# Kernel optimization log

Hardware: AMD Instinct MI355X
Metric: run time of the kernel (lower is better)

The kernel has to match this reference:

```python
import jax, jax.numpy as jnp
import numpy as np

D_MODEL = 1024
NUM_HEADS = 16
D_K = D_MODEL // NUM_HEADS


def setup_inputs() -> dict:
    key = jax.random.key(0)
    ks = jax.random.split(key, 12)
    B, L, D = 1, 4096, D_MODEL
    s = 1.0 / np.sqrt(D)
    return {
        "q": jax.random.normal(ks[0], (B, L, D), jnp.float32),
        "k": jax.random.normal(ks[1], (B, L, D), jnp.float32),
        "v": jax.random.normal(ks[2], (B, L, D), jnp.float32),
        "wq": jax.random.normal(ks[3], (D, D), jnp.float32) * s,
        "bq": jnp.zeros((D,), jnp.float32),
        "wk": jax.random.normal(ks[4], (D, D), jnp.float32) * s,
        "bk": jnp.zeros((D,), jnp.float32),
        "wv": jax.random.normal(ks[5], (D, D), jnp.float32) * s,
        "bv": jnp.zeros((D,), jnp.float32),
        "wo": jax.random.normal(ks[6], (D, D), jnp.float32) * s,
        "bo": jnp.zeros((D,), jnp.float32),
    }


def reference(q, k, v, wq, bq, wk, bk, wv, bv, wo, bo):
    B, L, D = q.shape
    H, dk = NUM_HEADS, D_K
    # linear projections then split heads: [B, L, D] -> [B, H, L, dk]
    def proj(x, w, b):
        return (x @ w.T + b).reshape(B, L, H, dk).transpose(0, 2, 1, 3)
    qh = proj(q, wq, bq)
    kh = proj(k, wk, bk)
    vh = proj(v, wv, bv)
    scores = jnp.einsum("bhqd,bhkd->bhqk", qh, kh) / jnp.sqrt(jnp.float32(dk))
    attn = jax.nn.softmax(scores, axis=-1)  # [B, H, L, L]
    out = jnp.einsum("bhqk,bhkd->bhqd", attn, vh)
    out = out.transpose(0, 2, 1, 3).reshape(B, L, D)
    return out @ wo.T + bo
```

## Files before the change

### kernel.cpp

```cpp
#include <hip/hip_runtime.h>
#include <hip/hip_bf16.h>
#include <stdint.h>


typedef __bf16 bf16_t;
typedef __bf16 bf16x8 __attribute__((ext_vector_type(8)));
typedef __bf16 bf16x4 __attribute__((ext_vector_type(4)));
typedef float f32x4 __attribute__((ext_vector_type(4)));
typedef unsigned short u16x8 __attribute__((ext_vector_type(8)));

#define MFMA_BF16 __builtin_amdgcn_mfma_f32_16x16x32_bf16

__device__ __forceinline__ void async_copy16(const void* g, void* lds) {
  __builtin_amdgcn_global_load_lds(
      (__attribute__((address_space(1))) void*)(uintptr_t)g,
      (__attribute__((address_space(3))) void*)lds, 16, 0, 0);
}

__global__ __launch_bounds__(256) void cast_f32_bf16(
    const float* __restrict__ s0, bf16_t* __restrict__ d0, int n0,
    const float* __restrict__ s1, bf16_t* __restrict__ d1, int n1,
    const float* __restrict__ s2, bf16_t* __restrict__ d2, int n2,
    const float* __restrict__ s3, bf16_t* __restrict__ d3, int n3,
    const float* __restrict__ s4, bf16_t* __restrict__ d4, int n4,
    const float* __restrict__ s5, bf16_t* __restrict__ d5, int n5,
    const float* __restrict__ s6, bf16_t* __restrict__ d6, int n6) {
  const float* s;
  bf16_t* d;
  int n;
  switch (blockIdx.z) {
    case 0: s = s0; d = d0; n = n0; break;
    case 1: s = s1; d = d1; n = n1; break;
    case 2: s = s2; d = d2; n = n2; break;
    case 3: s = s3; d = d3; n = n3; break;
    case 4: s = s4; d = d4; n = n4; break;
    case 5: s = s5; d = d5; n = n5; break;
    default: s = s6; d = d6; n = n6; break;
  }
  const int i = (blockIdx.x * 256 + threadIdx.x) * 8;
  if (i >= n) return;
  float4 a = *(const float4*)(s + i);
  float4 b = *(const float4*)(s + i + 4);
  bf16x8 o;
  o[0] = (bf16_t)a.x; o[1] = (bf16_t)a.y; o[2] = (bf16_t)a.z; o[3] = (bf16_t)a.w;
  o[4] = (bf16_t)b.x; o[5] = (bf16_t)b.y; o[6] = (bf16_t)b.z; o[7] = (bf16_t)b.w;
  *(bf16x8*)(d + i) = o;
}

template <typename CT>
__global__ __launch_bounds__(256) void gemm3_bt(
    const bf16_t* __restrict__ A0, const bf16_t* __restrict__ W0,
    const float* __restrict__ b0, CT* __restrict__ C0,
    const bf16_t* __restrict__ A1, const bf16_t* __restrict__ W1,
    const float* __restrict__ b1, CT* __restrict__ C1,
    const bf16_t* __restrict__ A2, const bf16_t* __restrict__ W2,
    const float* __restrict__ b2, CT* __restrict__ C2,
    int M, int N, int K) {
  const bf16_t *A, *W;
  const float* bias;
  CT* C;
  if (blockIdx.z == 0)      { A = A0; W = W0; bias = b0; C = C0; }
  else if (blockIdx.z == 1) { A = A1; W = W1; bias = b1; C = C1; }
  else                      { A = A2; W = W2; bias = b2; C = C2; }

  __shared__ bf16_t As[128][32];
  __shared__ bf16_t Bs[128][32];

  const int t = threadIdx.x;
  const int w = t >> 6, lane = t & 63;
  const int quad = lane >> 4, l16 = lane & 15;
  const int wr = w >> 1, wc = w & 1;
  const int m0 = blockIdx.x * 128;
  const int n0 = blockIdx.y * 128;
  const int srow = lane >> 2;
  const int scol = (lane & 3) * 8;

  f32x4 acc[4][4] = {};

  for (int k0 = 0; k0 < K; k0 += 32) {
    async_copy16(&A[(size_t)(m0 + (2 * w) * 16 + srow) * K + k0 + scol],
                 (char*)As + (2 * w) * 1024);
    async_copy16(&A[(size_t)(m0 + (2 * w + 1) * 16 + srow) * K + k0 + scol],
                 (char*)As + (2 * w + 1) * 1024);
    async_copy16(&W[(size_t)(n0 + (2 * w) * 16 + srow) * K + k0 + scol],
                 (char*)Bs + (2 * w) * 1024);
    async_copy16(&W[(size_t)(n0 + (2 * w + 1) * 16 + srow) * K + k0 + scol],
                 (char*)Bs + (2 * w + 1) * 1024);
    __syncthreads();

    bf16x8 af[4], bfr[4];
#pragma unroll
    for (int mt = 0; mt < 4; mt++)
      af[mt] = *(const bf16x8*)&As[wr * 64 + mt * 16 + l16][quad * 8];
#pragma unroll
    for (int nt = 0; nt < 4; nt++)
      bfr[nt] = *(const bf16x8*)&Bs[wc * 64 + nt * 16 + l16][quad * 8];
#pragma unroll
    for (int mt = 0; mt < 4; mt++)
#pragma unroll
      for (int nt = 0; nt < 4; nt++)
        acc[mt][nt] = MFMA_BF16(af[mt], bfr[nt], acc[mt][nt], 0, 0, 0);
    __syncthreads();
  }

#pragma unroll
  for (int nt = 0; nt < 4; nt++) {
    const int col = n0 + wc * 64 + nt * 16 + l16;
    const float bb = bias[col];
#pragma unroll
    for (int mt = 0; mt < 4; mt++) {
#pragma unroll
      for (int r = 0; r < 4; r++) {
        const int row = m0 + wr * 64 + mt * 16 + quad * 4 + r;
        C[(size_t)row * N + col] = (CT)(acc[mt][nt][r] + bb);
      }
    }
  }
}

__global__ __launch_bounds__(256) void frag_tile(
    const bf16_t* __restrict__ s0, bf16_t* __restrict__ d0,
    const bf16_t* __restrict__ s1, bf16_t* __restrict__ d1,
    const bf16_t* __restrict__ s2, bf16_t* __restrict__ d2) {
  const bf16_t* src;
  bf16_t* dst;
  const int z = blockIdx.z;
  if (z == 0)      { src = s0; dst = d0; }
  else if (z == 1) { src = s1; dst = d1; }
  else             { src = s2; dst = d2; }

  const int h = blockIdx.y;
  const int l0 = blockIdx.x * 64;
  const int t = threadIdx.x;

  __shared__ ushort Ts[64][72];

#pragma unroll
  for (int p = 0; p < 2; p++) {
    const int r = p * 32 + (t >> 3);
    const int c = (t & 7) * 8;
    float4 v = *(const float4*)(src + (size_t)(l0 + r) * 1024 + h * 64 + c);
    *(float4*)&Ts[r][c] = v;
  }
  __syncthreads();

  if (z < 2) {
    const float qscale = 0.125f * 1.44269504088896340736f;
#pragma unroll
    for (int p = 0; p < 2; p++) {
      const int gi = p * 256 + t;
      const int l16 = gi & 15, quad = (gi >> 4) & 3, kc = (gi >> 6) & 1;
      const int tl = gi >> 7;
      float4 v = *(const float4*)&Ts[tl * 16 + l16][kc * 32 + quad * 8];
      if (z == 0) {
        bf16x8 b = *(bf16x8*)&v;
#pragma unroll
        for (int e = 0; e < 8; e++) b[e] = (bf16_t)((float)b[e] * qscale);
        v = *(float4*)&b;
      }
      *(float4*)(dst + (size_t)(h * 256 + (l0 >> 4) + tl) * 1024 +
                 (size_t)(kc * 64 + quad * 16 + l16) * 8) = v;
    }
  } else {
#pragma unroll
    for (int p = 0; p < 2; p++) {
      const int gi = p * 256 + t;
      const int l16 = gi & 15, quad = (gi >> 4) & 3, kvc = (gi >> 6) & 1;
      const int dkt = gi >> 7;
      u16x8 tmp;
#pragma unroll
      for (int e = 0; e < 8; e++)
        tmp[e] = Ts[kvc * 32 + quad * 8 + e][dkt * 16 + l16];
      *(u16x8*)(dst + (size_t)(h * 256 + (l0 >> 6) * 4 + dkt) * 1024 +
                (size_t)(kvc * 64 + quad * 16 + l16) * 8) = tmp;
    }
  }
}

__global__ __launch_bounds__(256, 2) void flash_attn(
    const bf16_t* __restrict__ Qt, const bf16_t* __restrict__ Kt,
    const bf16_t* __restrict__ Vt, bf16_t* __restrict__ O, int L) {
  const int h = blockIdx.y;
  const int t = threadIdx.x;
  const int w = t >> 6, lane = t & 63;
  const int quad = lane >> 4, l16 = lane & 15;
  const int tq0 = blockIdx.x * 8 + w * 2;

  __shared__ bf16_t Kst[2][4096];
  __shared__ bf16_t Vst[2][4096];
  __shared__ bf16_t Pb[4][32][72];

  const size_t hb = (size_t)h * 256 * 1024;

  bf16x8 qa[2][2];
#pragma unroll
  for (int qt = 0; qt < 2; qt++)
#pragma unroll
    for (int kc = 0; kc < 2; kc++)
      qa[qt][kc] = *(const bf16x8*)(Qt + hb + (size_t)(tq0 + qt) * 1024 +
                                    kc * 512 + lane * 8);

#define STAGE(it_, buf_)                                                     \
  {                                                                          \
    const size_t cb = hb + (size_t)(it_) * 4096;                             \
    async_copy16(Kt + cb + (size_t)t * 8, (char*)&Kst[buf_][0] + w * 1024);  \
    async_copy16(Kt + cb + (size_t)(256 + t) * 8,                            \
                 (char*)&Kst[buf_][0] + 4096 + w * 1024);                    \
    async_copy16(Vt + cb + (size_t)t * 8, (char*)&Vst[buf_][0] + w * 1024);  \
    async_copy16(Vt + cb + (size_t)(256 + t) * 8,                            \
                 (char*)&Vst[buf_][0] + 4096 + w * 1024);                    \
  }

  STAGE(0, 0);

  f32x4 oT[2][4] = {};
  float ls[2] = {0.f, 0.f};

  const int NIT = L / 64;
  for (int it = 0; it < NIT; it++) {
    const int buf = it & 1;
    __syncthreads();
    if (it + 1 < NIT) STAGE(it + 1, buf ^ 1);

    bf16x8 kb[4][2], vb[4][2];
#pragma unroll
    for (int tt = 0; tt < 4; tt++)
#pragma unroll
      for (int kc = 0; kc < 2; kc++)
        kb[tt][kc] = *(const bf16x8*)((const char*)&Kst[buf][0] + tt * 2048 +
                                      kc * 1024 + lane * 16);
#pragma unroll
    for (int dkt = 0; dkt < 4; dkt++)
#pragma unroll
      for (int kvc = 0; kvc < 2; kvc++)
        vb[dkt][kvc] = *(const bf16x8*)((const char*)&Vst[buf][0] +
                                        dkt * 2048 + kvc * 1024 + lane * 16);

#pragma unroll
    for (int qt = 0; qt < 2; qt++) {
      f32x4 sT[4];
#pragma unroll
      for (int tt = 0; tt < 4; tt++) {
        f32x4 z = {0.f, 0.f, 0.f, 0.f};
        z = MFMA_BF16(kb[tt][0], qa[qt][0], z, 0, 0, 0);
        z = MFMA_BF16(kb[tt][1], qa[qt][1], z, 0, 0, 0);
        sT[tt] = z;
      }
#pragma unroll
      for (int tt = 0; tt < 4; tt++) {
        bf16x4 pk;
        float rs = 0.f;
#pragma unroll
        for (int r = 0; r < 4; r++) {
          const float p = __builtin_amdgcn_exp2f(sT[tt][r]);
          rs += p;
          pk[r] = (bf16_t)p;
        }
        ls[qt] += rs;
        *(bf16x4*)&Pb[w][qt * 16 + l16][tt * 16 + quad * 4] = pk;
      }
    }

#pragma unroll
    for (int qt = 0; qt < 2; qt++) {
      const bf16x8 pf0 = *(const bf16x8*)&Pb[w][qt * 16 + l16][quad * 8];
      const bf16x8 pf1 = *(const bf16x8*)&Pb[w][qt * 16 + l16][32 + quad * 8];
#pragma unroll
      for (int dkt = 0; dkt < 4; dkt++) {
        oT[qt][dkt] = MFMA_BF16(vb[dkt][0], pf0, oT[qt][dkt], 0, 0, 0);
        oT[qt][dkt] = MFMA_BF16(vb[dkt][1], pf1, oT[qt][dkt], 0, 0, 0);
      }
    }
  }
#undef STAGE

#pragma unroll
  for (int qt = 0; qt < 2; qt++) {
    float l = ls[qt];
    l += __shfl_xor(l, 16);
    l += __shfl_xor(l, 32);
    const float inv = 1.0f / l;
    const size_t row = (size_t)(tq0 + qt) * 16 + l16;
#pragma unroll
    for (int dkt = 0; dkt < 4; dkt++)
#pragma unroll
      for (int r = 0; r < 4; r++)
        O[row * 1024 + h * 64 + dkt * 16 + quad * 4 + r] =
            (bf16_t)(oT[qt][dkt][r] * inv);
  }
}

extern "C" void kernel_launch(void* const* d_in, const int* in_sizes, int n_in,
                              void* d_out, int out_size, void* d_ws,
                              size_t ws_size, hipStream_t stream) {
  const float* q  = (const float*)d_in[0];
  const float* k  = (const float*)d_in[1];
  const float* v  = (const float*)d_in[2];
  const float* wq = (const float*)d_in[3];
  const float* bq = (const float*)d_in[4];
  const float* wk = (const float*)d_in[5];
  const float* bk = (const float*)d_in[6];
  const float* wv = (const float*)d_in[7];
  const float* bv = (const float*)d_in[8];
  const float* wo = (const float*)d_in[9];
  const float* bo = (const float*)d_in[10];
  float* out = (float*)d_out;

  const int L = 4096, D = 1024;
  const int nLD = L * D;
  const int nDD = D * D;
  bf16_t* p = (bf16_t*)d_ws;
  bf16_t* qb  = p; p += nLD;
  bf16_t* kb  = p; p += nLD;
  bf16_t* vb  = p; p += nLD;
  bf16_t* wqb = p; p += nDD;
  bf16_t* wkb = p; p += nDD;
  bf16_t* wvb = p; p += nDD;
  bf16_t* wob = p; p += nDD;
  bf16_t* Qp  = p; p += nLD;
  bf16_t* Kp  = p; p += nLD;
  bf16_t* Vp  = p; p += nLD;
  bf16_t* Qt  = p; p += nLD;
  bf16_t* Kt  = p; p += nLD;
  bf16_t* Vt  = p; p += nLD;
  bf16_t* Op  = Qp;

  dim3 blk(256);
  cast_f32_bf16<<<dim3(nLD / (256 * 8), 1, 7), blk, 0, stream>>>(
      q, qb, nLD, k, kb, nLD, v, vb, nLD, wq, wqb, nDD, wk, wkb, nDD,
      wv, wvb, nDD, wo, wob, nDD);
  gemm3_bt<bf16_t><<<dim3(L / 128, D / 128, 3), blk, 0, stream>>>(
      qb, wqb, bq, Qp, kb, wkb, bk, Kp, vb, wvb, bv, Vp, L, D, D);
  frag_tile<<<dim3(L / 64, 16, 3), blk, 0, stream>>>(Qp, Qt, Kp, Kt, Vp, Vt);
  flash_attn<<<dim3(L / 128, 16), blk, 0, stream>>>(Qt, Kt, Vt, Op, L);
  gemm3_bt<float><<<dim3(L / 128, D / 128, 1), blk, 0, stream>>>(
      Op, wob, bo, out, Op, wob, bo, out, Op, wob, bo, out, L, D, D);
}
```

Before: 270.6 us.

## Use 512-thread attention blocks with one query tile per wave and XCD-aware head mapping

The flash attention kernel now launches 512-thread blocks of eight waves, each wave owning a single 16-row query tile instead of two. The shared K/V staging tile is therefore reused by more waves, and each thread issues half as many async copies. The 1D grid is remapped so each XCD (blockIdx mod 8) handles two heads, keeping that head's K/V in the XCD-local L2. Per-wave register pressure drops, but each wave now does less MFMA work per LDS load of K/V fragments, which could reduce compute density.

```diff
diff --git a/kernel.cpp b/kernel.cpp
--- a/kernel.cpp
+++ b/kernel.cpp
@@ -177,44 +177,43 @@
   }
 }
 
-__global__ __launch_bounds__(256, 2) void flash_attn(
+__global__ __launch_bounds__(512, 4) void flash_attn(
     const bf16_t* __restrict__ Qt, const bf16_t* __restrict__ Kt,
     const bf16_t* __restrict__ Vt, bf16_t* __restrict__ O, int L) {
-  const int h = blockIdx.y;
+  const int i = blockIdx.x;
+  const int xcd = i & 7;
+  const int slot = i >> 3;
+  const int h = xcd * 2 + (slot >> 5);
+  const int qblk = slot & 31;
+
   const int t = threadIdx.x;
   const int w = t >> 6, lane = t & 63;
   const int quad = lane >> 4, l16 = lane & 15;
-  const int tq0 = blockIdx.x * 8 + w * 2;
+  const int tq0 = qblk * 8 + w;
 
   __shared__ bf16_t Kst[2][4096];
   __shared__ bf16_t Vst[2][4096];
-  __shared__ bf16_t Pb[4][32][72];
+  __shared__ bf16_t Pb[8][16][72];
 
   const size_t hb = (size_t)h * 256 * 1024;
 
-  bf16x8 qa[2][2];
-#pragma unroll
-  for (int qt = 0; qt < 2; qt++)
-#pragma unroll
-    for (int kc = 0; kc < 2; kc++)
-      qa[qt][kc] = *(const bf16x8*)(Qt + hb + (size_t)(tq0 + qt) * 1024 +
-                                    kc * 512 + lane * 8);
+  bf16x8 qa[2];
+#pragma unroll
+  for (int kc = 0; kc < 2; kc++)
+    qa[kc] = *(const bf16x8*)(Qt + hb + (size_t)tq0 * 1024 + kc * 512 +
+                              lane * 8);
 
 #define STAGE(it_, buf_)                                                     \
   {                                                                          \
     const size_t cb = hb + (size_t)(it_) * 4096;                             \
     async_copy16(Kt + cb + (size_t)t * 8, (char*)&Kst[buf_][0] + w * 1024);  \
-    async_copy16(Kt + cb + (size_t)(256 + t) * 8,                            \
-                 (char*)&Kst[buf_][0] + 4096 + w * 1024);                    \
     async_copy16(Vt + cb + (size_t)t * 8, (char*)&Vst[buf_][0] + w * 1024);  \
-    async_copy16(Vt + cb + (size_t)(256 + t) * 8,                            \
-                 (char*)&Vst[buf_][0] + 4096 + w * 1024);                    \
   }
 
   STAGE(0, 0);
 
-  f32x4 oT[2][4] = {};
-  float ls[2] = {0.f, 0.f};
+  f32x4 oT[4] = {};
+  float ls = 0.f;
 
   const int NIT = L / 64;
   for (int it = 0; it < NIT; it++) {
@@ -236,58 +235,49 @@
         vb[dkt][kvc] = *(const bf16x8*)((const char*)&Vst[buf][0] +
                                         dkt * 2048 + kvc * 1024 + lane * 16);
 
-#pragma unroll
-    for (int qt = 0; qt < 2; qt++) {
-      f32x4 sT[4];
-#pragma unroll
-      for (int tt = 0; tt < 4; tt++) {
-        f32x4 z = {0.f, 0.f, 0.f, 0.f};
-        z = MFMA_BF16(kb[tt][0], qa[qt][0], z, 0, 0, 0);
-        z = MFMA_BF16(kb[tt][1], qa[qt][1], z, 0, 0, 0);
-        sT[tt] = z;
+    f32x4 sT[4];
+#pragma unroll
+    for (int tt = 0; tt < 4; tt++) {
+      f32x4 z = {0.f, 0.f, 0.f, 0.f};
+      z = MFMA_BF16(kb[tt][0], qa[0], z, 0, 0, 0);
+      z = MFMA_BF16(kb[tt][1], qa[1], z, 0, 0, 0);
+      sT[tt] = z;
+    }
+#pragma unroll
+    for (int tt = 0; tt < 4; tt++) {
+      bf16x4 pk;
+      float rs = 0.f;
+#pragma unroll
+      for (int r = 0; r < 4; r++) {
+        const float p = __builtin_amdgcn_exp2f(sT[tt][r]);
+        rs += p;
+        pk[r] = (bf16_t)p;
       }
-#pragma unroll
-      for (int tt = 0; tt < 4; tt++) {
-        bf16x4 pk;
-        float rs = 0.f;
-#pragma unroll
-        for (int r = 0; r < 4; r++) {
-          const float p = __builtin_amdgcn_exp2f(sT[tt][r]);
-          rs += p;
-          pk[r] = (bf16_t)p;
-        }
-        ls[qt] += rs;
-        *(bf16x4*)&Pb[w][qt * 16 + l16][tt * 16 + quad * 4] = pk;
-      }
-    }
-
-#pragma unroll
-    for (int qt = 0; qt < 2; qt++) {
-      const bf16x8 pf0 = *(const bf16x8*)&Pb[w][qt * 16 + l16][quad * 8];
-      const bf16x8 pf1 = *(const bf16x8*)&Pb[w][qt * 16 + l16][32 + quad * 8];
-#pragma unroll
-      for (int dkt = 0; dkt < 4; dkt++) {
-        oT[qt][dkt] = MFMA_BF16(vb[dkt][0], pf0, oT[qt][dkt], 0, 0, 0);
-        oT[qt][dkt] = MFMA_BF16(vb[dkt][1], pf1, oT[qt][dkt], 0, 0, 0);
-      }
+      ls += rs;
+      *(bf16x4*)&Pb[w][l16][tt * 16 + quad * 4] = pk;
+    }
+
+    const bf16x8 pf0 = *(const bf16x8*)&Pb[w][l16][quad * 8];
+    const bf16x8 pf1 = *(const bf16x8*)&Pb[w][l16][32 + quad * 8];
+#pragma unroll
+    for (int dkt = 0; dkt < 4; dkt++) {
+      oT[dkt] = MFMA_BF16(vb[dkt][0], pf0, oT[dkt], 0, 0, 0);
+      oT[dkt] = MFMA_BF16(vb[dkt][1], pf1, oT[dkt], 0, 0, 0);
     }
   }
 #undef STAGE
 
-#pragma unroll
-  for (int qt = 0; qt < 2; qt++) {
-    float l = ls[qt];
-    l += __shfl_xor(l, 16);
-    l += __shfl_xor(l, 32);
-    const float inv = 1.0f / l;
-    const size_t row = (size_t)(tq0 + qt) * 16 + l16;
-#pragma unroll
-    for (int dkt = 0; dkt < 4; dkt++)
-#pragma unroll
-      for (int r = 0; r < 4; r++)
-        O[row * 1024 + h * 64 + dkt * 16 + quad * 4 + r] =
-            (bf16_t)(oT[qt][dkt][r] * inv);
-  }
+  float l = ls;
+  l += __shfl_xor(l, 16);
+  l += __shfl_xor(l, 32);
+  const float inv = 1.0f / l;
+  const size_t row = (size_t)tq0 * 16 + l16;
+#pragma unroll
+  for (int dkt = 0; dkt < 4; dkt++)
+#pragma unroll
+    for (int r = 0; r < 4; r++)
+      O[row * 1024 + h * 64 + dkt * 16 + quad * 4 + r] =
+          (bf16_t)(oT[dkt][r] * inv);
 }
 
 extern "C" void kernel_launch(void* const* d_in, const int* in_sizes, int n_in,
@@ -332,7 +322,7 @@
   gemm3_bt<bf16_t><<<dim3(L / 128, D / 128, 3), blk, 0, stream>>>(
       qb, wqb, bq, Qp, kb, wkb, bk, Kp, vb, wvb, bv, Vp, L, D, D);
   frag_tile<<<dim3(L / 64, 16, 3), blk, 0, stream>>>(Qp, Qt, Kp, Kt, Vp, Vt);
-  flash_attn<<<dim3(L / 128, 16), blk, 0, stream>>>(Qt, Kt, Vt, Op, L);
+  flash_attn<<<dim3((L / 128) * 16), dim3(512), 0, stream>>>(Qt, Kt, Vt, Op, L);
   gemm3_bt<float><<<dim3(L / 128, D / 128, 1), blk, 0, stream>>>(
       Op, wob, bo, out, Op, wob, bo, out, Op, wob, bo, out, L, D, D);
 }
```

Result: no change. 271.5 us (+0.4%).
